# Optimization experiments

Measured on AMD Instinct MI355X. Metric: run time of the kernel, lower is better.

Reference implementation:

```python
import jax, jax.numpy as jnp
import numpy as np

NHEAD = 8
TOPKS = (8, 8)  # topk per level, coarse -> fine


def _to_bshd(x):
    # [B, C, H, W] -> [B, H*W, nhead, d]  (matches rearrange 'b c h w -> b (h w) c' + view)
    b, c, h, w = x.shape
    return jnp.transpose(x.reshape(b, c, h * w), (0, 2, 1)).reshape(b, h * w, NHEAD, c // NHEAD)


def _coarse_level(q, k, v, topk):
    b, c, h, w = k.shape
    d = c // NHEAD
    q_, k_, v_ = _to_bshd(q), _to_bshd(k), _to_bshd(v)
    temp = 1.0 / (d ** 0.5)
    A = jax.nn.softmax(jnp.einsum('nlhd,nshd->nlsh', q_, k_) * temp, axis=2)  # [b,L,S,h]
    _, idx = jax.lax.top_k(jnp.swapaxes(A, 2, 3), topk)  # [b,L,h,k]
    idx = jnp.swapaxes(idx, 2, 3)                        # [b,L,k,h]
    msg = jnp.einsum('nlsh,nshd->nlhd', A, v_)           # [b,L,h,d]
    topk_pos = jnp.stack([idx // w, idx % w])            # [2,b,L,k,h]
    return msg, topk_pos


def _fine_level(q, k, v, topk_pos, topk_prev, topk):
    b, c, h0, w0 = q.shape
    w1 = k.shape[3]
    d = c // NHEAD
    k_, v_ = _to_bshd(k), _to_bshd(v)
    H2, W2 = h0 // 2, w0 // 2
    L0 = H2 * W2
    # query grouped into 2x2 quads: [b, L0, 4, h, d]
    q_ = q.reshape(b, c, H2, 2, W2, 2).transpose(0, 2, 4, 3, 5, 1).reshape(b, L0, 4, NHEAD, d)
    tp = topk_pos * 2  # coarse positions -> fine grid
    cand = [(tp[0] + x) * w1 + tp[1] + y for x in (0, 1) for y in (0, 1)]
    t2 = topk_prev * 4
    idx = jnp.stack(cand, axis=3).reshape(b, L0, t2, NHEAD)  # [b,L,t2,h]
    idx_bh = idx.transpose(0, 3, 1, 2).reshape(b, NHEAD, L0 * t2)

    def gather(p):  # p: [b,S,h,d] -> gathered [b,L,t2,h,d]
        g = jnp.take_along_axis(jnp.swapaxes(p, 1, 2), idx_bh[..., None], axis=2)
        return g.reshape(b, NHEAD, L0, t2, d).transpose(0, 2, 3, 1, 4)

    tk, tv = gather(k_), gather(v_)
    temp = 1.0 / (d ** 0.5)
    A = jax.nn.softmax(jnp.einsum('blqhd,blthd->blqth', q_, tk) * temp, axis=3)  # [b,L,4,t2,h]
    _, ti = jax.lax.top_k(jnp.moveaxis(A, 3, 4), topk)  # [b,L,4,h,k]
    ti = jnp.moveaxis(ti, 4, 3)                         # [b,L,4,k,h]
    msg = jnp.einsum('blqth,blthd->blqhd', A, tv)       # [b,L,4,h,d]
    idx_b = jnp.broadcast_to(idx[:, :, None], (b, L0, 4, t2, NHEAD))
    gidx = jnp.take_along_axis(idx_b, ti, axis=3)       # [b,L,4,k,h] flat fine-grid indices
    gidx = gidx.reshape(b, H2, W2, 2, 2, topk, NHEAD).transpose(0, 1, 3, 2, 4, 5, 6)
    gidx = gidx.reshape(b, h0 * w0, topk, NHEAD)
    return msg, gidx


def _forward(q_fine, q_coarse, k_fine, k_coarse, v_fine, v_coarse, weight):
    msg0, topk_pos = _coarse_level(q_coarse, k_coarse, v_coarse, TOPKS[0])
    msg1, _ = _fine_level(q_fine, k_fine, v_fine, topk_pos, TOPKS[0], TOPKS[1])
    w = jax.nn.softmax(weight, axis=0)
    fm = msg0 * w[0]                  # [b,Lc,h,d]
    fm = fm[:, :, None] + msg1 * w[1]  # [b,Lc,4,h,d]
    b, Hc, Wc = q_coarse.shape[0], q_coarse.shape[2], q_coarse.shape[3]
    d = fm.shape[-1]
    # rearrange 'b (H W) (t1 t2) h d -> b (H t1 W t2) h d'
    fm = fm.reshape(b, Hc, Wc, 2, 2, NHEAD, d).transpose(0, 1, 3, 2, 4, 5, 6)
    return fm.reshape(b, Hc * Wc * 4, NHEAD, d)


def setup_inputs() -> dict:
    key = jax.random.key(0)
    ks = jax.random.split(key, 7)
    B, C = 4, 128
    return {
        'q_fine': jax.random.normal(ks[0], (B, C, 64, 64), jnp.float32),
        'q_coarse': jax.random.normal(ks[1], (B, C, 32, 32), jnp.float32),
        'k_fine': jax.random.normal(ks[2], (B, C, 64, 64), jnp.float32),
        'k_coarse': jax.random.normal(ks[3], (B, C, 32, 32), jnp.float32),
        'v_fine': jax.random.normal(ks[4], (B, C, 64, 64), jnp.float32),
        'v_coarse': jax.random.normal(ks[5], (B, C, 32, 32), jnp.float32),
        'weight': jax.random.normal(ks[6], (2,), jnp.float32),
    }


def reference(q_fine, q_coarse, k_fine, k_coarse, v_fine, v_coarse, weight):
    return _forward(q_fine, q_coarse, k_fine, k_coarse, v_fine, v_coarse, weight)
```

## Files before the change

### kernel.cpp

```cpp
#include <hip/hip_runtime.h>
#include <stdint.h>

#define TEMP 0.25f

static __device__ __forceinline__ uint32_t f2b_bits(float f){
    union { float f; uint32_t i; } x; x.f = f;
    uint32_t u = x.i;
    return (u + 0x7FFFu + ((u >> 16) & 1u)) >> 16;
}
static __device__ __forceinline__ float bl(uint32_t u){
    union { uint32_t i; float f; } x; x.i = u << 16; return x.f;
}
static __device__ __forceinline__ float bh(uint32_t u){
    union { uint32_t i; float f; } x; x.i = u & 0xffff0000u; return x.f;
}

__global__ __launch_bounds__(512, 2)
void coarse_kernel(const float* __restrict__ qc, const float* __restrict__ kc,
                   const float* __restrict__ vc, float* __restrict__ msg0,
                   int* __restrict__ topk_out)
{
    const int ltile = blockIdx.x;
    const int h     = blockIdx.y;
    const int b     = blockIdx.z;
    const int tid   = threadIdx.x;
    const int lane  = tid & 63;
    const int wv    = tid >> 6;
    const int lbase = ltile * 32;

    __shared__ float sKV[16 * 1024];

    const size_t base = (size_t)(b * 128 + h * 16) * 1024;

    {
        const float4* gK = (const float4*)(kc + base);
        float4* lK = (float4*)sKV;
        #pragma unroll
        for (int i = 0; i < 8; ++i) lK[tid + 512 * i] = gK[tid + 512 * i];
    }

    float qreg[4];
    {
        int dq = lane & 15;
        #pragma unroll
        for (int li = 0; li < 4; ++li){
            int l = lbase + wv * 4 + li;
            qreg[li] = qc[base + (size_t)dq * 1024 + l] * TEMP;
        }
    }
    __syncthreads();

    float p[4][16];
    #pragma unroll
    for (int li = 0; li < 4; ++li)
        #pragma unroll
        for (int j = 0; j < 16; ++j) p[li][j] = 0.f;

    #pragma unroll
    for (int dch = 0; dch < 16; ++dch){
        float kf[16];
        #pragma unroll
        for (int ch = 0; ch < 4; ++ch){
            float4 kv = *(const float4*)&sKV[dch * 1024 + ch * 256 + (lane << 2)];
            kf[ch*4+0] = kv.x; kf[ch*4+1] = kv.y;
            kf[ch*4+2] = kv.z; kf[ch*4+3] = kv.w;
        }
        float qs[4];
        #pragma unroll
        for (int li = 0; li < 4; ++li) qs[li] = __shfl(qreg[li], dch);
        #pragma unroll
        for (int li = 0; li < 4; ++li)
            #pragma unroll
            for (int j = 0; j < 16; ++j)
                p[li][j] = fmaf(qs[li], kf[j], p[li][j]);
    }

    float invs[4];
    #pragma unroll
    for (int li = 0; li < 4; ++li){
        float m = p[li][0];
        #pragma unroll
        for (int j = 1; j < 16; ++j) m = fmaxf(m, p[li][j]);
        #pragma unroll
        for (int off = 32; off > 0; off >>= 1) m = fmaxf(m, __shfl_xor(m, off));
        float s = 0.f;
        #pragma unroll
        for (int j = 0; j < 16; ++j){ p[li][j] = __expf(p[li][j] - m); s += p[li][j]; }
        #pragma unroll
        for (int off = 32; off > 0; off >>= 1) s += __shfl_xor(s, off);
        invs[li] = 1.0f / s;
    }

    __syncthreads();
    {
        const float4* gV = (const float4*)(vc + base);
        float4* lV = (float4*)sKV;
        #pragma unroll
        for (int i = 0; i < 8; ++i) lV[tid + 512 * i] = gV[tid + 512 * i];
    }
    __syncthreads();

    float outv = 0.f;
    #pragma unroll
    for (int dd = 0; dd < 16; ++dd){
        float vf[16];
        #pragma unroll
        for (int ch = 0; ch < 4; ++ch){
            float4 vv = *(const float4*)&sKV[dd * 1024 + ch * 256 + (lane << 2)];
            vf[ch*4+0] = vv.x; vf[ch*4+1] = vv.y;
            vf[ch*4+2] = vv.z; vf[ch*4+3] = vv.w;
        }
        float a[4];
        #pragma unroll
        for (int li = 0; li < 4; ++li){
            float s = 0.f;
            #pragma unroll
            for (int j = 0; j < 16; ++j) s = fmaf(p[li][j], vf[j], s);
            a[li] = s;
        }
        #pragma unroll
        for (int off = 32; off > 0; off >>= 1)
            #pragma unroll
            for (int li = 0; li < 4; ++li) a[li] += __shfl_xor(a[li], off);
        #pragma unroll
        for (int li = 0; li < 4; ++li)
            outv = (lane == li * 16 + dd) ? a[li] * invs[li] : outv;
    }
    {
        int li = lane >> 4, dd = lane & 15;
        int l = lbase + wv * 4 + li;
        msg0[(size_t)((b * 1024 + l) * 8 + h) * 16 + dd] = outv;
    }

    const int lanebase = lane << 4;
    int mytk = 0;
    for (int r = 0; r < 8; ++r){
        float bv[4]; int bi[4];
        #pragma unroll
        for (int li = 0; li < 4; ++li){
            float v0[8]; int j0[8];
            #pragma unroll
            for (int k = 0; k < 8; ++k){
                bool g = p[li][2*k+1] > p[li][2*k];
                v0[k] = g ? p[li][2*k+1] : p[li][2*k];
                j0[k] = g ? 2*k+1 : 2*k;
            }
            float v1[4]; int j1[4];
            #pragma unroll
            for (int k = 0; k < 4; ++k){
                bool g = v0[2*k+1] > v0[2*k];
                v1[k] = g ? v0[2*k+1] : v0[2*k];
                j1[k] = g ? j0[2*k+1] : j0[2*k];
            }
            float v2[2]; int j2[2];
            #pragma unroll
            for (int k = 0; k < 2; ++k){
                bool g = v1[2*k+1] > v1[2*k];
                v2[k] = g ? v1[2*k+1] : v1[2*k];
                j2[k] = g ? j1[2*k+1] : j1[2*k];
            }
            bool g3 = v2[1] > v2[0];
            bv[li] = g3 ? v2[1] : v2[0];
            bi[li] = lanebase | (g3 ? j2[1] : j2[0]);
        }
        #pragma unroll
        for (int off = 32; off > 0; off >>= 1){
            #pragma unroll
            for (int li = 0; li < 4; ++li){
                float ov = __shfl_xor(bv[li], off);
                int   oi = __shfl_xor(bi[li], off);
                bool g = (ov > bv[li]) || (ov == bv[li] && oi < bi[li]);
                bv[li] = g ? ov : bv[li];
                bi[li] = g ? oi : bi[li];
            }
        }
        #pragma unroll
        for (int li = 0; li < 4; ++li){
            #pragma unroll
            for (int j = 0; j < 16; ++j)
                p[li][j] = (bi[li] == (lanebase | j)) ? -1.0f : p[li][j];
            mytk = (lane == li * 8 + r) ? bi[li] : mytk;
        }
    }
    if (lane < 32){
        int li = lane >> 3, r = lane & 7;
        int jw = mytk & 15, lw = mytk >> 4;
        int s = ((jw >> 2) << 8) | (lw << 2) | (jw & 3);
        int l = lbase + wv * 4 + li;
        topk_out[((b * 1024 + l) * 8 + h) * 8 + r] = s;
    }
}

__global__ __launch_bounds__(256)
void pack_kernel(const float* __restrict__ kf, const float* __restrict__ vf,
                 const float* __restrict__ qf,
                 uint32_t* __restrict__ packed, float* __restrict__ qT)
{
    const int pt = blockIdx.x;
    const int b  = blockIdx.y;
    const int z  = blockIdx.z;
    const float* src = (z == 0) ? kf : (z == 1) ? vf : qf;
    const int tid = threadIdx.x;
    __shared__ float tile[64][129];
    const int pos0 = pt * 64;

    #pragma unroll
    for (int it = 0; it < 8; ++it){
        int task = it * 256 + tid;
        int ch = task >> 4, p4 = task & 15;
        float4 v = *(const float4*)(src + (size_t)(b * 128 + ch) * 4096 + pos0 + p4 * 4);
        tile[p4*4+0][ch] = v.x; tile[p4*4+1][ch] = v.y;
        tile[p4*4+2][ch] = v.z; tile[p4*4+3][ch] = v.w;
    }
    __syncthreads();

    if (z == 2){
        #pragma unroll
        for (int it = 0; it < 8; ++it){
            int task = it * 256 + tid;
            int p = task >> 5, c4 = task & 31;
            float4 v = make_float4(tile[p][c4*4+0], tile[p][c4*4+1],
                                   tile[p][c4*4+2], tile[p][c4*4+3]);
            *(float4*)(qT + ((size_t)(b * 4096) + pos0 + p) * 128 + c4 * 4) = v;
        }
    } else {
        const int x = pt;
        #pragma unroll
        for (int it = 0; it < 2; ++it){
            int task = it * 256 + tid;
            int h = task >> 6, y = task & 63;
            int pprime = ((x >> 1) * 32 + (y >> 1)) * 4 + (x & 1) * 2 + (y & 1);
            size_t line = (size_t)(b * 8 + h) * 4096 + pprime;
            uint32_t dw[8];
            #pragma unroll
            for (int i = 0; i < 8; ++i){
                uint32_t lo = f2b_bits(tile[y][h * 16 + 2 * i]);
                uint32_t hi = f2b_bits(tile[y][h * 16 + 2 * i + 1]);
                dw[i] = lo | (hi << 16);
            }
            uint4* dst4 = (uint4*)packed + line * 4 + z * 2;
            dst4[0] = make_uint4(dw[0], dw[1], dw[2], dw[3]);
            dst4[1] = make_uint4(dw[4], dw[5], dw[6], dw[7]);
        }
    }
}

__global__ __launch_bounds__(256)
void fine_kernel(const float* __restrict__ qf, const float* __restrict__ kf,
                 const float* __restrict__ vf,
                 const float* __restrict__ qTg, const uint32_t* __restrict__ packed,
                 int transposed,
                 const float* __restrict__ wt,
                 const int* __restrict__ topk_in, const float* __restrict__ msg0,
                 float* __restrict__ out)
{
    const int l0 = blockIdx.x;
    const int b  = blockIdx.y;
    const int tid = threadIdx.x;

    __shared__ float vT[8][16][34];
    __shared__ float qT[8][4][16];
    __shared__ float pT[8][4][32];
    __shared__ int tkS[8][8];

    if (tid < 64) tkS[tid >> 3][tid & 7] =
        topk_in[((b * 1024 + l0) * 8 + (tid >> 3)) * 8 + (tid & 7)];
    __syncthreads();

    const int i = l0 >> 5, j = l0 & 31;
    const int hh = tid >> 5;
    const int t  = tid & 31;
    const int kk = t >> 2, cp = t & 3;

    float k[16];
    {
        int s = tkS[hh][kk];
        if (transposed){
            const uint4* pk = (const uint4*)packed;
            size_t line = (size_t)(b * 8 + hh) * 4096 + s * 4 + cp;
            uint4 a0 = pk[line*4+0], a1 = pk[line*4+1];
            uint4 a2 = pk[line*4+2], a3 = pk[line*4+3];
            k[0]=bl(a0.x);  k[1]=bh(a0.x);  k[2]=bl(a0.y);  k[3]=bh(a0.y);
            k[4]=bl(a0.z);  k[5]=bh(a0.z);  k[6]=bl(a0.w);  k[7]=bh(a0.w);
            k[8]=bl(a1.x);  k[9]=bh(a1.x);  k[10]=bl(a1.y); k[11]=bh(a1.y);
            k[12]=bl(a1.z); k[13]=bh(a1.z); k[14]=bl(a1.w); k[15]=bh(a1.w);
            vT[hh][0][t]=bl(a2.x);  vT[hh][1][t]=bh(a2.x);
            vT[hh][2][t]=bl(a2.y);  vT[hh][3][t]=bh(a2.y);
            vT[hh][4][t]=bl(a2.z);  vT[hh][5][t]=bh(a2.z);
            vT[hh][6][t]=bl(a2.w);  vT[hh][7][t]=bh(a2.w);
            vT[hh][8][t]=bl(a3.x);  vT[hh][9][t]=bh(a3.x);
            vT[hh][10][t]=bl(a3.y); vT[hh][11][t]=bh(a3.y);
            vT[hh][12][t]=bl(a3.z); vT[hh][13][t]=bh(a3.z);
            vT[hh][14][t]=bl(a3.w); vT[hh][15][t]=bh(a3.w);
        } else {
            int pos = (2 * (s >> 5) + (cp >> 1)) * 64 + 2 * (s & 31) + (cp & 1);
            size_t gb = (size_t)(b * 128 + hh * 16) * 4096 + pos;
            #pragma unroll
            for (int ch = 0; ch < 16; ++ch){
                k[ch] = kf[gb + (size_t)ch * 4096];
                vT[hh][ch][t] = vf[gb + (size_t)ch * 4096];
            }
        }
    }
    if (tid < 128){
        int qh = tid >> 4, aq = (tid >> 2) & 3, c4 = tid & 3;
        int qpos = (2 * i + (aq >> 1)) * 64 + 2 * j + (aq & 1);
        if (transposed){
            float4 u = *(const float4*)(qTg + ((size_t)(b * 4096) + qpos) * 128 + qh * 16 + c4 * 4);
            qT[qh][aq][c4*4+0] = u.x * TEMP;
            qT[qh][aq][c4*4+1] = u.y * TEMP;
            qT[qh][aq][c4*4+2] = u.z * TEMP;
            qT[qh][aq][c4*4+3] = u.w * TEMP;
        } else {
            #pragma unroll
            for (int c = 0; c < 4; ++c)
                qT[qh][aq][c4*4+c] =
                    qf[(size_t)(b * 128 + qh * 16 + c4 * 4 + c) * 4096 + qpos] * TEMP;
        }
    }
    __syncthreads();

    {
        float sc[4] = {0.f, 0.f, 0.f, 0.f};
        #pragma unroll
        for (int dch = 0; dch < 16; ++dch){
            float kv = k[dch];
            #pragma unroll
            for (int q = 0; q < 4; ++q) sc[q] = fmaf(qT[hh][q][dch], kv, sc[q]);
        }
        #pragma unroll
        for (int q = 0; q < 4; ++q){
            float m = sc[q];
            #pragma unroll
            for (int off = 16; off > 0; off >>= 1) m = fmaxf(m, __shfl_xor(m, off, 32));
            float e = __expf(sc[q] - m);
            float s = e;
            #pragma unroll
            for (int off = 16; off > 0; off >>= 1) s += __shfl_xor(s, off, 32);
            pT[hh][q][t] = e / s;
        }
    }
    __syncthreads();

    {
        float w0 = wt[0], w1 = wt[1];
        float mx = fmaxf(w0, w1);
        float e0 = __expf(w0 - mx), e1 = __expf(w1 - mx);
        float w0f = e0 / (e0 + e1), w1f = e1 / (e0 + e1);

        int q0 = (tid >> 4) & 1;
        int dd = tid & 15;
        float a0 = 0.f, a1 = 0.f;
        #pragma unroll
        for (int tt = 0; tt < 16; ++tt){
            float v0 = vT[hh][dd][tt * 2], v1 = vT[hh][dd][tt * 2 + 1];
            float2 pA = *(const float2*)&pT[hh][q0][tt * 2];
            float2 pB = *(const float2*)&pT[hh][q0 + 2][tt * 2];
            a0 = fmaf(pA.x, v0, a0); a0 = fmaf(pA.y, v1, a0);
            a1 = fmaf(pB.x, v0, a1); a1 = fmaf(pB.y, v1, a1);
        }
        float m0 = msg0[(size_t)((b * 1024 + l0) * 8 + hh) * 16 + dd];
        float o0 = w0f * m0 + w1f * a0;
        float o1 = w0f * m0 + w1f * a1;
        int posA = (2 * i) * 64 + 2 * j + q0;
        int posB = (2 * i + 1) * 64 + 2 * j + q0;
        out[(size_t)((b * 4096 + posA) * 8 + hh) * 16 + dd] = o0;
        out[(size_t)((b * 4096 + posB) * 8 + hh) * 16 + dd] = o1;
    }
}

extern "C" void kernel_launch(void* const* d_in, const int* in_sizes, int n_in,
                              void* d_out, int out_size, void* d_ws, size_t ws_size,
                              hipStream_t stream)
{
    (void)in_sizes; (void)n_in; (void)out_size;

    const float* q_fine   = (const float*)d_in[0];
    const float* q_coarse = (const float*)d_in[1];
    const float* k_fine   = (const float*)d_in[2];
    const float* k_coarse = (const float*)d_in[3];
    const float* v_fine   = (const float*)d_in[4];
    const float* v_coarse = (const float*)d_in[5];
    const float* weight   = (const float*)d_in[6];

    const size_t MB = 1024 * 1024;
    float*    msg0   = (float*)d_ws;
    int*      topk   = (int*)((char*)d_ws + 2 * MB);
    float*    qT     = (float*)((char*)d_ws + 3 * MB);
    uint32_t* packed = (uint32_t*)((char*)d_ws + 11 * MB);
    const int doT = (ws_size >= 19 * MB) ? 1 : 0;

    if (doT){
        dim3 gt(64, 4, 3);
        pack_kernel<<<gt, dim3(256), 0, stream>>>(k_fine, v_fine, q_fine, packed, qT);
    }

    dim3 g1(32, 8, 4);
    coarse_kernel<<<g1, dim3(512), 0, stream>>>(q_coarse, k_coarse, v_coarse, msg0, topk);

    dim3 g2(1024, 4);
    fine_kernel<<<g2, dim3(256), 0, stream>>>(q_fine, k_fine, v_fine,
                                              qT, packed, doT,
                                              weight, topk, msg0, (float*)d_out);
}
```

Measured before the change: 219.9 us.

## Move coarse attention onto bf16 MFMA with split-precision operand packing

Adds a pack kernel that splits coarse K and V into bf16 hi/lo parts laid out for MFMA fragments. A new coarse kernel then computes QK^T and PV with mfma_f32_16x16x32_bf16, using three-term (K) and two-term (V) bf16 splits to keep near-fp32 accuracy. Softmax and top-k are reduced across four waves through shared memory, with a final merge of per-wave top-8 lists. The path only runs when the workspace is at least 25 MB; otherwise the old scalar kernel is used. It adds an extra launch and extra workspace traffic, and top-k tie ordering may drift slightly from the fp32 result.

```diff
diff --git a/kernel.cpp b/kernel.cpp
--- a/kernel.cpp
+++ b/kernel.cpp
@@ -2,17 +2,247 @@
 #include <stdint.h>
 
 #define TEMP 0.25f
+
+typedef unsigned short u16;
+typedef short v8s __attribute__((ext_vector_type(8)));
+typedef float v4f __attribute__((ext_vector_type(4)));
 
 static __device__ __forceinline__ uint32_t f2b_bits(float f){
     union { float f; uint32_t i; } x; x.f = f;
     uint32_t u = x.i;
     return (u + 0x7FFFu + ((u >> 16) & 1u)) >> 16;
 }
+static __device__ __forceinline__ float b2f(u16 u){
+    union { uint32_t i; float f; } x; x.i = ((uint32_t)u) << 16; return x.f;
+}
 static __device__ __forceinline__ float bl(uint32_t u){
     union { uint32_t i; float f; } x; x.i = u << 16; return x.f;
 }
 static __device__ __forceinline__ float bh(uint32_t u){
     union { uint32_t i; float f; } x; x.i = u & 0xffff0000u; return x.f;
+}
+static __device__ __forceinline__ uint4 pack8(const uint32_t* e){
+    return make_uint4(e[0] | (e[1] << 16), e[2] | (e[3] << 16),
+                      e[4] | (e[5] << 16), e[6] | (e[7] << 16));
+}
+union U8S { uint4 u; v8s s; };
+static __device__ __forceinline__ v8s asv8s(uint4 u){ U8S x; x.u = u; return x.s; }
+static __device__ __forceinline__ v8s swapq(v8s v){
+    union { v8s s; int i[4]; } x; x.s = v;
+    #pragma unroll
+    for (int k = 0; k < 4; ++k) x.i[k] = __shfl_xor(x.i[k], 32);
+    return x.s;
+}
+
+__global__ __launch_bounds__(256)
+void pack_coarse(const float* __restrict__ kc, const float* __restrict__ vc,
+                 uint4* __restrict__ KP1, uint4* __restrict__ KP3,
+                 uint4* __restrict__ VP1)
+{
+    const int bh = blockIdx.x;
+    const int kv = blockIdx.y;
+    const int b = bh >> 3, h = bh & 7;
+    const int tid = threadIdx.x;
+    const size_t sbase = (size_t)(b * 128 + h * 16) * 1024;
+    const size_t fbase = (size_t)bh * 64 * 64;
+
+    #pragma unroll
+    for (int it = 0; it < 16; ++it){
+        int task = it * 256 + tid;
+        int kt = task >> 6, ln = task & 63;
+        int quad = ln >> 4, col = ln & 15;
+        if (kv == 0){
+            uint32_t e1[8], e3[8];
+            #pragma unroll
+            for (int j = 0; j < 8; ++j){
+                int dch = (quad & 1) * 8 + j;
+                float x = kc[sbase + (size_t)dch * 1024 + kt * 16 + col];
+                uint32_t u0 = f2b_bits(x);
+                float r1 = x - b2f((u16)u0);
+                uint32_t u1 = f2b_bits(r1);
+                float r2 = r1 - b2f((u16)u1);
+                uint32_t u2 = f2b_bits(r2);
+                e1[j] = (quad < 2) ? u0 : u1;
+                e3[j] = (quad < 2) ? u2 : u0;
+            }
+            KP1[fbase + kt * 64 + ln] = pack8(e1);
+            KP3[fbase + kt * 64 + ln] = pack8(e3);
+        } else {
+            uint32_t e[8];
+            #pragma unroll
+            for (int j = 0; j < 8; ++j){
+                int key = kt * 16 + (quad & 1) * 8 + j;
+                float x = vc[sbase + (size_t)col * 1024 + key];
+                uint32_t u0 = f2b_bits(x);
+                uint32_t u1 = f2b_bits(x - b2f((u16)u0));
+                e[j] = (quad < 2) ? u0 : u1;
+            }
+            VP1[fbase + kt * 64 + ln] = pack8(e);
+        }
+    }
+}
+
+__global__ __launch_bounds__(256)
+void coarse_mfma(const float* __restrict__ qc,
+                 const uint4* __restrict__ KP1, const uint4* __restrict__ KP3,
+                 const uint4* __restrict__ VP1,
+                 float* __restrict__ msg0, int* __restrict__ topk_out)
+{
+    const int ltile = blockIdx.x;
+    const int h = blockIdx.y, b = blockIdx.z;
+    const int bh = b * 8 + h;
+    const int tid = threadIdx.x, lane = tid & 63, wv = tid >> 6;
+    const int quad = lane >> 4, col = lane & 15;
+    const int lbase = ltile * 16;
+
+    __shared__ float tls[4][320];
+    __shared__ float rred[2][4][16];
+    __shared__ float pvred[4][16][16];
+    __shared__ float tkv[4][16][8];
+    __shared__ int   tki[4][16][8];
+
+    v8s a1, a3;
+    {
+        int row = lbase + col;
+        int dch0 = (quad & 1) * 8;
+        #pragma unroll
+        for (int j = 0; j < 8; ++j){
+            float x = qc[(size_t)(b * 128 + h * 16 + dch0 + j) * 1024 + row] * TEMP;
+            uint32_t u0 = f2b_bits(x);
+            float r1 = x - b2f((u16)u0);
+            uint32_t u1 = f2b_bits(r1);
+            float r2 = r1 - b2f((u16)u1);
+            uint32_t u2 = f2b_bits(r2);
+            a1[j] = (short)(quad < 2 ? u0 : u1);
+            a3[j] = (short)(quad < 2 ? u0 : u2);
+        }
+    }
+
+    const size_t fbase = (size_t)bh * 64 * 64;
+    v4f sc[16];
+    #pragma unroll
+    for (int kt = 0; kt < 16; ++kt){
+        int ktg = wv * 16 + kt;
+        v8s b1 = asv8s(KP1[fbase + (size_t)ktg * 64 + lane]);
+        v8s b3 = asv8s(KP3[fbase + (size_t)ktg * 64 + lane]);
+        v8s b2 = swapq(b1);
+        v4f c = {0.f, 0.f, 0.f, 0.f};
+        c = __builtin_amdgcn_mfma_f32_16x16x32_bf16(a1, b1, c, 0, 0, 0);
+        c = __builtin_amdgcn_mfma_f32_16x16x32_bf16(a1, b2, c, 0, 0, 0);
+        c = __builtin_amdgcn_mfma_f32_16x16x32_bf16(a3, b3, c, 0, 0, 0);
+        sc[kt] = c;
+    }
+
+    #pragma unroll
+    for (int r = 0; r < 4; ++r){
+        float m = sc[0][r];
+        #pragma unroll
+        for (int kt = 1; kt < 16; ++kt) m = fmaxf(m, sc[kt][r]);
+        #pragma unroll
+        for (int off = 1; off < 16; off <<= 1) m = fmaxf(m, __shfl_xor(m, off));
+        if (col == 0) rred[0][wv][quad * 4 + r] = m;
+    }
+    __syncthreads();
+    #pragma unroll
+    for (int r = 0; r < 4; ++r){
+        int row = quad * 4 + r;
+        float m = fmaxf(fmaxf(rred[0][0][row], rred[0][1][row]),
+                        fmaxf(rred[0][2][row], rred[0][3][row]));
+        #pragma unroll
+        for (int kt = 0; kt < 16; ++kt) sc[kt][r] = __expf(sc[kt][r] - m);
+    }
+    #pragma unroll
+    for (int r = 0; r < 4; ++r){
+        float s = 0.f;
+        #pragma unroll
+        for (int kt = 0; kt < 16; ++kt) s += sc[kt][r];
+        #pragma unroll
+        for (int off = 1; off < 16; off <<= 1) s += __shfl_xor(s, off);
+        if (col == 0) rred[1][wv][quad * 4 + r] = s;
+    }
+
+    v4f acc = {0.f, 0.f, 0.f, 0.f};
+    float* tw = tls[wv];
+    const int ab = (lane & 15) * 20 + (quad & 1) * 8;
+    #pragma unroll
+    for (int kt = 0; kt < 16; ++kt){
+        #pragma unroll
+        for (int r = 0; r < 4; ++r) tw[(quad * 4 + r) * 20 + col] = sc[kt][r];
+        __builtin_amdgcn_s_waitcnt(0xC07F);
+        v8s ap;
+        #pragma unroll
+        for (int j = 0; j < 8; ++j){
+            float x = tw[ab + j];
+            uint32_t u0 = f2b_bits(x);
+            uint32_t u1 = f2b_bits(x - b2f((u16)u0));
+            ap[j] = (short)(quad < 2 ? u0 : u1);
+        }
+        int ktg = wv * 16 + kt;
+        v8s bv1 = asv8s(VP1[fbase + (size_t)ktg * 64 + lane]);
+        v8s bv2 = swapq(bv1);
+        acc = __builtin_amdgcn_mfma_f32_16x16x32_bf16(ap, bv1, acc, 0, 0, 0);
+        acc = __builtin_amdgcn_mfma_f32_16x16x32_bf16(ap, bv2, acc, 0, 0, 0);
+    }
+    #pragma unroll
+    for (int r = 0; r < 4; ++r) pvred[wv][quad * 4 + r][col] = acc[r];
+    __syncthreads();
+
+    {
+        int row = tid >> 4, dd = tid & 15;
+        float v = pvred[0][row][dd] + pvred[1][row][dd] +
+                  pvred[2][row][dd] + pvred[3][row][dd];
+        float s = rred[1][0][row] + rred[1][1][row] +
+                  rred[1][2][row] + rred[1][3][row];
+        msg0[((size_t)((b * 1024 + lbase + row) * 8 + h)) * 16 + dd] = v / s;
+    }
+
+    #pragma unroll
+    for (int r = 0; r < 4; ++r){
+        int row = quad * 4 + r;
+        #pragma unroll
+        for (int rnd = 0; rnd < 8; ++rnd){
+            float bv = sc[0][r]; int bk = 0;
+            #pragma unroll
+            for (int kt = 1; kt < 16; ++kt){
+                bool g = sc[kt][r] > bv;
+                bv = g ? sc[kt][r] : bv; bk = g ? kt : bk;
+            }
+            int bi = bk * 16 + col;
+            #pragma unroll
+            for (int off = 1; off < 16; off <<= 1){
+                float ov = __shfl_xor(bv, off);
+                int   oi = __shfl_xor(bi, off);
+                bool g = (ov > bv) || (ov == bv && oi < bi);
+                bv = g ? ov : bv; bi = g ? oi : bi;
+            }
+            if ((bi & 15) == col){
+                int ktw = bi >> 4;
+                #pragma unroll
+                for (int kt = 0; kt < 16; ++kt)
+                    if (kt == ktw) sc[kt][r] = -1.0f;
+            }
+            if (col == rnd){ tkv[wv][row][rnd] = bv; tki[wv][row][rnd] = wv * 256 + bi; }
+        }
+    }
+    __syncthreads();
+    if (tid < 16){
+        int row = tid;
+        int* tp = topk_out + (((b * 1024 + lbase + row) * 8 + h) * 8);
+        int p[4] = {0, 0, 0, 0};
+        #pragma unroll
+        for (int rnd = 0; rnd < 8; ++rnd){
+            float bv = -3.0f; int bw = 0, bi = 0x7fffffff;
+            #pragma unroll
+            for (int w = 0; w < 4; ++w){
+                float v = tkv[w][row][p[w]];
+                int   i = tki[w][row][p[w]];
+                bool g = (v > bv) || (v == bv && i < bi);
+                bv = g ? v : bv; bi = g ? i : bi; bw = g ? w : bw;
+            }
+            tp[rnd] = bi;
+            p[bw]++;
+        }
+    }
 }
 
 __global__ __launch_bounds__(512, 2)
@@ -21,24 +251,18 @@
                    int* __restrict__ topk_out)
 {
     const int ltile = blockIdx.x;
-    const int h     = blockIdx.y;
-    const int b     = blockIdx.z;
-    const int tid   = threadIdx.x;
-    const int lane  = tid & 63;
-    const int wv    = tid >> 6;
+    const int h = blockIdx.y, b = blockIdx.z;
+    const int tid = threadIdx.x;
+    const int lane = tid & 63, wv = tid >> 6;
     const int lbase = ltile * 32;
-
     __shared__ float sKV[16 * 1024];
-
     const size_t base = (size_t)(b * 128 + h * 16) * 1024;
-
     {
         const float4* gK = (const float4*)(kc + base);
         float4* lK = (float4*)sKV;
         #pragma unroll
         for (int i = 0; i < 8; ++i) lK[tid + 512 * i] = gK[tid + 512 * i];
     }
-
     float qreg[4];
     {
         int dq = lane & 15;
@@ -49,21 +273,18 @@
         }
     }
     __syncthreads();
-
     float p[4][16];
     #pragma unroll
     for (int li = 0; li < 4; ++li)
         #pragma unroll
         for (int j = 0; j < 16; ++j) p[li][j] = 0.f;
-
     #pragma unroll
     for (int dch = 0; dch < 16; ++dch){
         float kf[16];
         #pragma unroll
         for (int ch = 0; ch < 4; ++ch){
             float4 kv = *(const float4*)&sKV[dch * 1024 + ch * 256 + (lane << 2)];
-            kf[ch*4+0] = kv.x; kf[ch*4+1] = kv.y;
-            kf[ch*4+2] = kv.z; kf[ch*4+3] = kv.w;
+            kf[ch*4+0] = kv.x; kf[ch*4+1] = kv.y; kf[ch*4+2] = kv.z; kf[ch*4+3] = kv.w;
         }
         float qs[4];
         #pragma unroll
@@ -71,10 +292,8 @@
         #pragma unroll
         for (int li = 0; li < 4; ++li)
             #pragma unroll
-            for (int j = 0; j < 16; ++j)
-                p[li][j] = fmaf(qs[li], kf[j], p[li][j]);
-    }
-
+            for (int j = 0; j < 16; ++j) p[li][j] = fmaf(qs[li], kf[j], p[li][j]);
+    }
     float invs[4];
     #pragma unroll
     for (int li = 0; li < 4; ++li){
@@ -90,7 +309,6 @@
         for (int off = 32; off > 0; off >>= 1) s += __shfl_xor(s, off);
         invs[li] = 1.0f / s;
     }
-
     __syncthreads();
     {
         const float4* gV = (const float4*)(vc + base);
@@ -99,7 +317,6 @@
         for (int i = 0; i < 8; ++i) lV[tid + 512 * i] = gV[tid + 512 * i];
     }
     __syncthreads();
-
     float outv = 0.f;
     #pragma unroll
     for (int dd = 0; dd < 16; ++dd){
@@ -107,8 +324,7 @@
         #pragma unroll
         for (int ch = 0; ch < 4; ++ch){
             float4 vv = *(const float4*)&sKV[dd * 1024 + ch * 256 + (lane << 2)];
-            vf[ch*4+0] = vv.x; vf[ch*4+1] = vv.y;
-            vf[ch*4+2] = vv.z; vf[ch*4+3] = vv.w;
+            vf[ch*4+0] = vv.x; vf[ch*4+1] = vv.y; vf[ch*4+2] = vv.z; vf[ch*4+3] = vv.w;
         }
         float a[4];
         #pragma unroll
@@ -131,7 +347,6 @@
         int l = lbase + wv * 4 + li;
         msg0[(size_t)((b * 1024 + l) * 8 + h) * 16 + dd] = outv;
     }
-
     const int lanebase = lane << 4;
     int mytk = 0;
     for (int r = 0; r < 8; ++r){
@@ -388,18 +603,29 @@
     int*      topk   = (int*)((char*)d_ws + 2 * MB);
     float*    qT     = (float*)((char*)d_ws + 3 * MB);
     uint32_t* packed = (uint32_t*)((char*)d_ws + 11 * MB);
+    uint4*    KP1    = (uint4*)((char*)d_ws + 19 * MB);
+    uint4*    KP3    = (uint4*)((char*)d_ws + 21 * MB);
+    uint4*    VP1    = (uint4*)((char*)d_ws + 23 * MB);
     const int doT = (ws_size >= 19 * MB) ? 1 : 0;
+    const int doM = (ws_size >= 25 * MB) ? 1 : 0;
+
+    if (doM){
+        pack_coarse<<<dim3(32, 2), dim3(256), 0, stream>>>(k_coarse, v_coarse,
+                                                           KP1, KP3, VP1);
+        coarse_mfma<<<dim3(64, 8, 4), dim3(256), 0, stream>>>(q_coarse, KP1, KP3, VP1,
+                                                              msg0, topk);
+    } else {
+        coarse_kernel<<<dim3(32, 8, 4), dim3(512), 0, stream>>>(q_coarse, k_coarse,
+                                                                v_coarse, msg0, topk);
+    }
 
     if (doT){
-        dim3 gt(64, 4, 3);
-        pack_kernel<<<gt, dim3(256), 0, stream>>>(k_fine, v_fine, q_fine, packed, qT);
-    }
-
-    dim3 g1(32, 8, 4);
-    coarse_kernel<<<g1, dim3(512), 0, stream>>>(q_coarse, k_coarse, v_coarse, msg0, topk);
-
-    dim3 g2(1024, 4);
-    fine_kernel<<<g2, dim3(256), 0, stream>>>(q_fine, k_fine, v_fine,
-                                              qT, packed, doT,
-                                              weight, topk, msg0, (float*)d_out);
-}
+        pack_kernel<<<dim3(64, 4, 3), dim3(256), 0, stream>>>(k_fine, v_fine, q_fine,
+                                                              packed, qT);
+    }
+
+    fine_kernel<<<dim3(1024, 4), dim3(256), 0, stream>>>(q_fine, k_fine, v_fine,
+                                                         qT, packed, doT,
+                                                         weight, topk, msg0,
+                                                         (float*)d_out);
+}
```

Result: slower. 233.0 us (+5.9%).
